# Kernel tuning notes

Measured on AMD Instinct MI355X. Metric: run time of the kernel, lower is better.

The kernel has to match this reference:

```python
import jax, jax.numpy as jnp
import numpy as np

ALPHA = 0.2  # leaky_relu negative slope (init arg `alpha`)


def setup_inputs() -> dict:
    key = jax.random.key(0)
    k0, k1, k2, k3, k4 = jax.random.split(key, 5)
    B, N, F_IN, F_OUT, H = 8, 512, 128, 64, 1  # n_heads must be 1 (torch.cat constraint)
    h = jax.random.normal(k0, (B, N, F_IN), jnp.float32)
    edge_features = jax.random.normal(k1, (B, N, N, F_OUT), jnp.float32)
    # learned params (xavier-ish scale)
    W = jax.random.normal(k2, (H, F_IN, F_OUT), jnp.float32) * 0.1
    U = jax.random.normal(k3, (H, F_OUT), jnp.float32) * 0.1
    a = jax.random.normal(k4, (H, 2 * F_OUT + 1), jnp.float32) * 0.1
    return {"h": h, "edge_features": edge_features, "W": W, "U": U, "a": a}


def reference(h, edge_features, W, U, a):
    # h: [B,N,F_in], edge_features: [B,N,N,F_out], W: [H,F_in,F_out], U: [H,F_out], a: [H,2*F_out+1]
    F_OUT = W.shape[-1]
    Wh = jnp.einsum('bni,hio->bhno', h, W)  # [B,H,N,F_out]
    # Split additive attention vector instead of materializing the O(N^2, 2F+1) concat:
    # sum(cat([Wh_i, Wh_j, edge_t]) * a) == Wh_i@a_i + Wh_j@a_j + edge_t*a_e
    a_i = a[:, :F_OUT]            # [H,F_out]
    a_j = a[:, F_OUT:2 * F_OUT]   # [H,F_out]
    a_e = a[:, 2 * F_OUT]         # [H]
    e_i = jnp.einsum('bhno,ho->bhn', Wh, a_i)  # score contribution of node i
    e_j = jnp.einsum('bhno,ho->bhn', Wh, a_j)  # score contribution of node j
    edge_s = jnp.einsum('bijo,ho->bhij', edge_features, U)  # [B,H,N,N] (H=1)
    e = e_i[:, :, :, None] + e_j[:, :, None, :] + edge_s * a_e[None, :, None, None]
    e = jnp.where(e >= 0, e, ALPHA * e)  # leaky_relu
    attn = jax.nn.softmax(e, axis=3)     # softmax over neighbors j (dropout p=0 -> identity)
    h_prime = jnp.einsum('bhij,bhjo->bhio', attn, Wh)  # [B,H,N,F_out]
    B, H, N, _ = h_prime.shape
    # concat=True: [B,N,H*F_out]
    return jnp.transpose(h_prime, (0, 2, 1, 3)).reshape(B, N, H * F_OUT)
```

## Files before the change

### kernel.cpp

```cpp
#include <hip/hip_runtime.h>

#define BN 8
#define NN 512
#define FIN 128
#define FOUT 64
#define ALPHA 0.2f

__global__ __launch_bounds__(64) void wh_kernel(
    const float* __restrict__ h, const float* __restrict__ W,
    const float* __restrict__ a,
    float* __restrict__ Wh, float* __restrict__ e_i, float* __restrict__ e_j) {
    int bn = blockIdx.x;
    int o  = threadIdx.x;
    __shared__ float hrow[FIN];
    hrow[o]      = h[bn * FIN + o];
    hrow[o + 64] = h[bn * FIN + 64 + o];
    __syncthreads();
    float acc = 0.f;
#pragma unroll 8
    for (int i = 0; i < FIN; ++i)
        acc = fmaf(hrow[i], W[i * FOUT + o], acc);
    Wh[bn * FOUT + o] = acc;
    float pi = acc * a[o];
    float pj = acc * a[FOUT + o];
#pragma unroll
    for (int off = 32; off >= 1; off >>= 1) {
        pi += __shfl_xor(pi, off, 64);
        pj += __shfl_xor(pj, off, 64);
    }
    if (o == 0) { e_i[bn] = pi; e_j[bn] = pj; }
}

__global__ __launch_bounds__(256) void attn_kernel(
    const float* __restrict__ edge, const float* __restrict__ U,
    const float* __restrict__ a, const float* __restrict__ Wh,
    const float* __restrict__ e_i, const float* __restrict__ e_j,
    float* __restrict__ out) {
    int bi   = blockIdx.x;
    int b    = bi >> 9;
    int tid  = threadIdx.x;
    int lane = tid & 63;
    int wave = tid >> 6;

    __shared__ float s_lds[NN];
    __shared__ float ej_lds[NN];
    __shared__ float red[8];
    __shared__ float accbuf[4][FOUT];

    ej_lds[tid]       = e_j[(b << 9) + tid];
    ej_lds[tid + 256] = e_j[(b << 9) + tid + 256];

    float a_e = a[2 * FOUT];
    float eiv = e_i[bi];
    int   sub = lane & 15;
    float4 Uv = ((const float4*)U)[sub];
    const float4* erow = (const float4*)(edge + (size_t)bi * (NN * FOUT));
    int jbase = (wave << 2) + (lane >> 4);
    __syncthreads();

#pragma unroll 4
    for (int it = 0; it < 32; ++it) {
        int j = (it << 4) + jbase;
        float4 ef = erow[(j << 4) + sub];
        float p = ef.x * Uv.x + ef.y * Uv.y + ef.z * Uv.z + ef.w * Uv.w;
        p += __shfl_xor(p, 8, 16);
        p += __shfl_xor(p, 4, 16);
        p += __shfl_xor(p, 2, 16);
        p += __shfl_xor(p, 1, 16);
        if (sub == 0) {
            float s = eiv + ej_lds[j] + a_e * p;
            s_lds[j] = (s >= 0.f) ? s : (ALPHA * s);
        }
    }
    __syncthreads();

    float m = fmaxf(s_lds[tid], s_lds[tid + 256]);
#pragma unroll
    for (int off = 32; off >= 1; off >>= 1) m = fmaxf(m, __shfl_xor(m, off, 64));
    if (lane == 0) red[wave] = m;
    __syncthreads();
    m = fmaxf(fmaxf(red[0], red[1]), fmaxf(red[2], red[3]));
    float v0 = expf(s_lds[tid] - m);
    float v1 = expf(s_lds[tid + 256] - m);
    float ssum = v0 + v1;
    s_lds[tid] = v0;
    s_lds[tid + 256] = v1;
#pragma unroll
    for (int off = 32; off >= 1; off >>= 1) ssum += __shfl_xor(ssum, off, 64);
    if (lane == 0) red[4 + wave] = ssum;
    __syncthreads();
    float inv = 1.0f / (red[4] + red[5] + red[6] + red[7]);

    int o = tid & 63, chunk = tid >> 6;
    const float* WhB = Wh + (((size_t)b) << 9) * FOUT;
    float acc = 0.f;
    int j0 = chunk << 7;
#pragma unroll 8
    for (int j = j0; j < j0 + 128; ++j)
        acc = fmaf(s_lds[j], WhB[(j << 6) + o], acc);
    accbuf[chunk][o] = acc;
    __syncthreads();
    if (chunk == 0) {
        float r = (accbuf[0][o] + accbuf[1][o] + accbuf[2][o] + accbuf[3][o]) * inv;
        out[((size_t)bi << 6) + o] = r;
    }
}

extern "C" void kernel_launch(void* const* d_in, const int* in_sizes, int n_in,
                              void* d_out, int out_size, void* d_ws, size_t ws_size,
                              hipStream_t stream) {
    const float* h    = (const float*)d_in[0];
    const float* edge = (const float*)d_in[1];
    const float* W    = (const float*)d_in[2];
    const float* U    = (const float*)d_in[3];
    const float* a    = (const float*)d_in[4];
    float* out = (float*)d_out;

    float* Wh  = (float*)d_ws;
    float* e_i = Wh + BN * NN * FOUT;
    float* e_j = e_i + BN * NN;

    wh_kernel<<<BN * NN, 64, 0, stream>>>(h, W, a, Wh, e_i, e_j);
    attn_kernel<<<BN * NN, 256, 0, stream>>>(edge, U, a, Wh, e_i, e_j, out);
}
```

Baseline: 697.2 us.

## Give each thread whole edge rows with nontemporal vector loads, vectorize Wh aggregation

The edge-score phase now assigns one full 64-float edge row to each thread (two rows per thread). Each thread issues 16 unrolled nontemporal float4 loads per row and reduces them in registers. This replaces the 16-lane shuffle reduction and the scattered per-j writes to shared memory, and keeps many more loads in flight per thread. The price is that each wave load instruction now touches 64 separate rows instead of one coalesced contiguous segment. The Wh aggregation uses float4 loads with a cross-lane shuffle reduction, U moves into shared memory, and launch bounds ask for 4 blocks per SIMD.

```diff
diff --git a/kernel.cpp b/kernel.cpp
--- a/kernel.cpp
+++ b/kernel.cpp
@@ -5,6 +5,8 @@
 #define FIN 128
 #define FOUT 64
 #define ALPHA 0.2f
+
+typedef float f32x4 __attribute__((ext_vector_type(4)));
 
 __global__ __launch_bounds__(64) void wh_kernel(
     const float* __restrict__ h, const float* __restrict__ W,
@@ -31,7 +33,7 @@
     if (o == 0) { e_i[bn] = pi; e_j[bn] = pj; }
 }
 
-__global__ __launch_bounds__(256) void attn_kernel(
+__global__ __launch_bounds__(256, 4) void attn_kernel(
     const float* __restrict__ edge, const float* __restrict__ U,
     const float* __restrict__ a, const float* __restrict__ Wh,
     const float* __restrict__ e_i, const float* __restrict__ e_j,
@@ -42,36 +44,36 @@
     int lane = tid & 63;
     int wave = tid >> 6;
 
+    __shared__ f32x4 Uf4[16];
     __shared__ float s_lds[NN];
-    __shared__ float ej_lds[NN];
     __shared__ float red[8];
     __shared__ float accbuf[4][FOUT];
 
-    ej_lds[tid]       = e_j[(b << 9) + tid];
-    ej_lds[tid + 256] = e_j[(b << 9) + tid + 256];
-
+    if (tid < 16) Uf4[tid] = ((const f32x4*)U)[tid];
     float a_e = a[2 * FOUT];
     float eiv = e_i[bi];
-    int   sub = lane & 15;
-    float4 Uv = ((const float4*)U)[sub];
-    const float4* erow = (const float4*)(edge + (size_t)bi * (NN * FOUT));
-    int jbase = (wave << 2) + (lane >> 4);
+    float ej0 = e_j[(b << 9) + tid];
+    float ej1 = e_j[(b << 9) + 256 + tid];
     __syncthreads();
 
-#pragma unroll 4
-    for (int it = 0; it < 32; ++it) {
-        int j = (it << 4) + jbase;
-        float4 ef = erow[(j << 4) + sub];
-        float p = ef.x * Uv.x + ef.y * Uv.y + ef.z * Uv.z + ef.w * Uv.w;
-        p += __shfl_xor(p, 8, 16);
-        p += __shfl_xor(p, 4, 16);
-        p += __shfl_xor(p, 2, 16);
-        p += __shfl_xor(p, 1, 16);
-        if (sub == 0) {
-            float s = eiv + ej_lds[j] + a_e * p;
-            s_lds[j] = (s >= 0.f) ? s : (ALPHA * s);
-        }
+    const f32x4* r0 = (const f32x4*)(edge + (size_t)bi * (NN * FOUT)) + tid * 16;
+    const f32x4* r1 = r0 + 256 * 16;
+    f32x4 acc0 = {0.f, 0.f, 0.f, 0.f};
+    f32x4 acc1 = {0.f, 0.f, 0.f, 0.f};
+#pragma unroll
+    for (int k = 0; k < 16; ++k) {
+        f32x4 u  = Uf4[k];
+        f32x4 x0 = __builtin_nontemporal_load(&r0[k]);
+        f32x4 x1 = __builtin_nontemporal_load(&r1[k]);
+        acc0 += x0 * u;
+        acc1 += x1 * u;
     }
+    float p0 = (acc0.x + acc0.y) + (acc0.z + acc0.w);
+    float p1 = (acc1.x + acc1.y) + (acc1.z + acc1.w);
+    float s0 = eiv + ej0 + a_e * p0;
+    float s1 = eiv + ej1 + a_e * p1;
+    s_lds[tid]       = (s0 >= 0.f) ? s0 : (ALPHA * s0);
+    s_lds[tid + 256] = (s1 >= 0.f) ? s1 : (ALPHA * s1);
     __syncthreads();
 
     float m = fmaxf(s_lds[tid], s_lds[tid + 256]);
@@ -83,7 +85,7 @@
     float v0 = expf(s_lds[tid] - m);
     float v1 = expf(s_lds[tid + 256] - m);
     float ssum = v0 + v1;
-    s_lds[tid] = v0;
+    s_lds[tid]       = v0;
     s_lds[tid + 256] = v1;
 #pragma unroll
     for (int off = 32; off >= 1; off >>= 1) ssum += __shfl_xor(ssum, off, 64);
@@ -91,18 +93,29 @@
     __syncthreads();
     float inv = 1.0f / (red[4] + red[5] + red[6] + red[7]);
 
-    int o = tid & 63, chunk = tid >> 6;
-    const float* WhB = Wh + (((size_t)b) << 9) * FOUT;
-    float acc = 0.f;
-    int j0 = chunk << 7;
+    int o4 = lane & 15;
+    int jg = lane >> 4;
+    const f32x4* Wh4 = (const f32x4*)(Wh + (((size_t)b) << 9) * FOUT);
+    f32x4 acc = {0.f, 0.f, 0.f, 0.f};
 #pragma unroll 8
-    for (int j = j0; j < j0 + 128; ++j)
-        acc = fmaf(s_lds[j], WhB[(j << 6) + o], acc);
-    accbuf[chunk][o] = acc;
+    for (int it = 0; it < 32; ++it) {
+        int j = (it << 4) + (wave << 2) + jg;
+        float pj = s_lds[j];
+        f32x4 w4 = Wh4[(j << 4) + o4];
+        acc.x = fmaf(pj, w4.x, acc.x);
+        acc.y = fmaf(pj, w4.y, acc.y);
+        acc.z = fmaf(pj, w4.z, acc.z);
+        acc.w = fmaf(pj, w4.w, acc.w);
+    }
+    acc.x += __shfl_xor(acc.x, 16, 64); acc.x += __shfl_xor(acc.x, 32, 64);
+    acc.y += __shfl_xor(acc.y, 16, 64); acc.y += __shfl_xor(acc.y, 32, 64);
+    acc.z += __shfl_xor(acc.z, 16, 64); acc.z += __shfl_xor(acc.z, 32, 64);
+    acc.w += __shfl_xor(acc.w, 16, 64); acc.w += __shfl_xor(acc.w, 32, 64);
+    if (lane < 16) ((f32x4*)accbuf)[(wave << 4) + o4] = acc;
     __syncthreads();
-    if (chunk == 0) {
-        float r = (accbuf[0][o] + accbuf[1][o] + accbuf[2][o] + accbuf[3][o]) * inv;
-        out[((size_t)bi << 6) + o] = r;
+    if (tid < 64) {
+        float r = (accbuf[0][tid] + accbuf[1][tid] + accbuf[2][tid] + accbuf[3][tid]) * inv;
+        out[((size_t)bi << 6) + tid] = r;
     }
 }
 
```

After: 952.6 us. 1.37x slower.
